# Optimization experiments

Measured on AMD Instinct MI355X. Metric: run time of the kernel, lower is better.

The kernel has to match this reference:

```python
import jax, jax.numpy as jnp
import numpy as np

D_MODEL = 2048
N_HEADS = 16
HEAD_DIM = D_MODEL // N_HEADS
SCALE = HEAD_DIM ** -0.5


def setup_inputs() -> dict:
    key = jax.random.key(0)
    ks = jax.random.split(key, 9)
    B, L, D = 4, 4096, D_MODEL
    s = 1.0 / np.sqrt(D)
    inp = {"x": jax.random.normal(ks[0], (B, L, D), dtype=jnp.float32)}
    inp["Wq"] = jax.random.normal(ks[1], (D, D), dtype=jnp.float32) * s
    inp["bq"] = jnp.zeros((D,), dtype=jnp.float32)
    inp["Wk"] = jax.random.normal(ks[2], (D, D), dtype=jnp.float32) * s
    inp["bk"] = jnp.zeros((D,), dtype=jnp.float32)
    inp["Wv"] = jax.random.normal(ks[3], (D, D), dtype=jnp.float32) * s
    inp["bv"] = jnp.zeros((D,), dtype=jnp.float32)
    inp["Wo"] = jax.random.normal(ks[4], (D, D), dtype=jnp.float32) * s
    inp["bo"] = jnp.zeros((D,), dtype=jnp.float32)
    return inp


def reference(x, Wq, bq, Wk, bk, Wv, bv, Wo, bo):
    B, L, D = x.shape
    H, Hd = N_HEADS, HEAD_DIM
    # projections (torch Linear: x @ W.T + b)
    q = jnp.einsum('bld,ed->ble', x, Wq) + bq
    k = jnp.einsum('bld,ed->ble', x, Wk) + bk
    v = jnp.einsum('bld,ed->ble', x, Wv) + bv
    phi_q = jax.nn.elu(q) + 1.0
    phi_k = jax.nn.elu(k) + 1.0
    # (B, L, H, Hd)
    phi_q = phi_q.reshape(B, L, H, Hd)
    phi_k = phi_k.reshape(B, L, H, Hd)
    v = v.reshape(B, L, H, Hd)
    # elementwise prefix sum over sequence dim
    kv_sum = jnp.cumsum(phi_k * v, axis=1)  # (B, L, H, Hd)
    context = (phi_q * kv_sum).reshape(B, L, D) * SCALE
    return jnp.einsum('bld,ed->ble', context, Wo) + bo
```

## Files before the change

### kernel.cpp

```cpp
#include <hip/hip_runtime.h>
#include <hip/hip_bf16.h>
#include <cstdint>
#include <cstddef>

typedef __bf16 bf16x8 __attribute__((ext_vector_type(8)));
typedef __bf16 bf16x4 __attribute__((ext_vector_type(4)));
typedef float  f32x4  __attribute__((ext_vector_type(4)));

#define D_MODEL 2048
#define SEQ     4096
#define BATCH   4
#define M_TOK   (BATCH * SEQ)
#define ATTN_SCALE 0.08838834764831845f

#define BM 128
#define BN 128
#define BK 64

#define NSEG   64
#define SEGLEN (SEQ / NSEG)

__device__ __forceinline__ void async_load16(const void* g, void* l) {
    __builtin_amdgcn_global_load_lds(
        (const __attribute__((address_space(1))) unsigned int*)g,
        (__attribute__((address_space(3))) unsigned int*)l,
        16, 0, 0);
}

__global__ __launch_bounds__(256) void k_cast_bf16(const float* __restrict__ in,
                                                   __bf16* __restrict__ out,
                                                   int n8) {
    int i = blockIdx.x * 256 + threadIdx.x;
    if (i >= n8) return;
    const float4* in4 = (const float4*)in;
    float4 a = in4[2 * i];
    float4 b = in4[2 * i + 1];
    bf16x8 o;
    o[0] = (__bf16)a.x; o[1] = (__bf16)a.y; o[2] = (__bf16)a.z; o[3] = (__bf16)a.w;
    o[4] = (__bf16)b.x; o[5] = (__bf16)b.y; o[6] = (__bf16)b.z; o[7] = (__bf16)b.w;
    ((bf16x8*)out)[i] = o;
}

__global__ __launch_bounds__(256) void k_cast_w4(const float* __restrict__ w0,
                                                 const float* __restrict__ w1,
                                                 const float* __restrict__ w2,
                                                 const float* __restrict__ w3,
                                                 __bf16* __restrict__ out, int n8) {
    const float* srcs[4] = {w0, w1, w2, w3};
    const float* in = srcs[blockIdx.y];
    __bf16* o = out + (size_t)blockIdx.y * (size_t)n8 * 8;
    int i = blockIdx.x * 256 + threadIdx.x;
    if (i >= n8) return;
    const float4* in4 = (const float4*)in;
    float4 a = in4[2 * i];
    float4 b = in4[2 * i + 1];
    bf16x8 v;
    v[0] = (__bf16)a.x; v[1] = (__bf16)a.y; v[2] = (__bf16)a.z; v[3] = (__bf16)a.w;
    v[4] = (__bf16)b.x; v[5] = (__bf16)b.y; v[6] = (__bf16)b.z; v[7] = (__bf16)b.w;
    ((bf16x8*)o)[i] = v;
}

template <int PHI, typename OUT_T>
__device__ __forceinline__ void gemm_bt(const __bf16* __restrict__ A,
                                        const __bf16* __restrict__ Bm,
                                        const float* __restrict__ bias,
                                        OUT_T* __restrict__ C,
                                        int K, int N) {
    __shared__ __align__(16) __bf16 As[BM * BK];
    __shared__ __align__(16) __bf16 Bs[BN * BK];

    const int tid  = threadIdx.x;
    const int lane = tid & 63;
    const int wave = tid >> 6;
    const int waveM = wave & 1;
    const int waveN = wave >> 1;
    const long bm = (long)blockIdx.y * BM;
    const long bn = (long)blockIdx.x * BN;

    const int srow  = tid >> 3;
    const int sphys = tid & 7;
    const __bf16* gA[4]; const __bf16* gB[4];
    __bf16* lA[4]; __bf16* lB[4];
#pragma unroll
    for (int q = 0; q < 4; q++) {
        int r  = q * 32 + srow;
        int cb = (sphys ^ (r & 7)) * 8;
        gA[q] = A  + (bm + r) * (long)K + cb;
        gB[q] = Bm + (bn + r) * (long)K + cb;
        lA[q] = As + q * 2048 + tid * 8;
        lB[q] = Bs + q * 2048 + tid * 8;
    }

    const int mrow = waveM * 64 + (lane & 15);
    const int nrow = waveN * 64 + (lane & 15);
    const int ksel = lane >> 4;

    f32x4 acc[4][4] = {};

    for (int k0 = 0; k0 < K; k0 += BK) {
#pragma unroll
        for (int q = 0; q < 4; q++) async_load16(gA[q] + k0, lA[q]);
#pragma unroll
        for (int q = 0; q < 4; q++) async_load16(gB[q] + k0, lB[q]);
        __syncthreads();

#pragma unroll
        for (int s = 0; s < 2; s++) {
            bf16x8 af[4], bfr[4];
#pragma unroll
            for (int i = 0; i < 4; i++) {
                int r = mrow + i * 16;
                int p = (s * 4 + ksel) ^ (r & 7);
                af[i] = *(const bf16x8*)(As + r * 64 + p * 8);
            }
#pragma unroll
            for (int j = 0; j < 4; j++) {
                int r = nrow + j * 16;
                int p = (s * 4 + ksel) ^ (r & 7);
                bfr[j] = *(const bf16x8*)(Bs + r * 64 + p * 8);
            }
#pragma unroll
            for (int i = 0; i < 4; i++)
#pragma unroll
                for (int j = 0; j < 4; j++)
                    acc[i][j] = __builtin_amdgcn_mfma_f32_16x16x32_bf16(
                        af[i], bfr[j], acc[i][j], 0, 0, 0);
        }
        __syncthreads();
    }

    const int r0 = (lane >> 4) * 4;
    const int cn = lane & 15;
#pragma unroll
    for (int i = 0; i < 4; i++) {
        long mg = bm + waveM * 64 + i * 16 + r0;
#pragma unroll
        for (int j = 0; j < 4; j++) {
            long ng = bn + waveN * 64 + j * 16 + cn;
            float bia = bias[ng];
#pragma unroll
            for (int r = 0; r < 4; r++) {
                float v = acc[i][j][r] + bia;
                if (PHI) v = (v > 0.f) ? (v + 1.f) : __expf(v);
                C[(mg + r) * (long)N + ng] = (OUT_T)v;
            }
        }
    }
}

__global__ __launch_bounds__(256) void k_gemm_qkv(
    const __bf16* __restrict__ xb,
    const __bf16* __restrict__ wq, const __bf16* __restrict__ wk, const __bf16* __restrict__ wv,
    const float* __restrict__ bq, const float* __restrict__ bk, const float* __restrict__ bv,
    __bf16* __restrict__ oq, __bf16* __restrict__ ok, __bf16* __restrict__ ov) {
    const int z = blockIdx.z;
    const __bf16* W = (z == 0) ? wq : (z == 1) ? wk : wv;
    const float*  b = (z == 0) ? bq : (z == 1) ? bk : bv;
    __bf16*       o = (z == 0) ? oq : (z == 1) ? ok : ov;
    if (z < 2)
        gemm_bt<1, __bf16>(xb, W, b, o, D_MODEL, D_MODEL);
    else
        gemm_bt<0, __bf16>(xb, W, b, o, D_MODEL, D_MODEL);
}

__global__ __launch_bounds__(256) void k_gemm_out(
    const __bf16* __restrict__ ctx, const __bf16* __restrict__ wo,
    const float* __restrict__ bo, float* __restrict__ out) {
    gemm_bt<0, float>(ctx, wo, bo, out, D_MODEL, D_MODEL);
}

__global__ __launch_bounds__(256) void k_scan_partial(
    const __bf16* __restrict__ phik, const __bf16* __restrict__ v,
    float* __restrict__ partial) {
    const int b  = blockIdx.z;
    const int s  = blockIdx.y;
    const int c0 = blockIdx.x * 1024 + threadIdx.x * 4;
    long base = ((long)b * SEQ + (long)s * SEGLEN) * D_MODEL + c0;
    const bf16x4* pk = (const bf16x4*)(phik + base);
    const bf16x4* pv = (const bf16x4*)(v + base);
    float s0 = 0, s1 = 0, s2 = 0, s3 = 0;
    for (int l = 0; l < SEGLEN; l++) {
        bf16x4 a = *pk, w = *pv;
        s0 += (float)a[0] * (float)w[0];
        s1 += (float)a[1] * (float)w[1];
        s2 += (float)a[2] * (float)w[2];
        s3 += (float)a[3] * (float)w[3];
        pk += D_MODEL / 4; pv += D_MODEL / 4;
    }
    *(float4*)(partial + ((long)(b * NSEG + s)) * D_MODEL + c0) = make_float4(s0, s1, s2, s3);
}

__global__ __launch_bounds__(256) void k_scan_apply(
    const __bf16* __restrict__ phiq,
    __bf16* phik_ctx,
    const __bf16* __restrict__ v,
    const float* __restrict__ partial) {
    const int b  = blockIdx.z;
    const int s  = blockIdx.y;
    const int c0 = blockIdx.x * 1024 + threadIdx.x * 4;
    float r0 = 0, r1 = 0, r2 = 0, r3 = 0;
    for (int sp = 0; sp < s; sp++) {
        float4 p = *(const float4*)(partial + ((long)(b * NSEG + sp)) * D_MODEL + c0);
        r0 += p.x; r1 += p.y; r2 += p.z; r3 += p.w;
    }
    long base = ((long)b * SEQ + (long)s * SEGLEN) * D_MODEL + c0;
    bf16x4* pk = (bf16x4*)(phik_ctx + base);
    const bf16x4* pv = (const bf16x4*)(v + base);
    const bf16x4* pq = (const bf16x4*)(phiq + base);
    for (int l = 0; l < SEGLEN; l++) {
        bf16x4 a = *pk, w = *pv, q = *pq;
        r0 += (float)a[0] * (float)w[0];
        r1 += (float)a[1] * (float)w[1];
        r2 += (float)a[2] * (float)w[2];
        r3 += (float)a[3] * (float)w[3];
        bf16x4 o;
        o[0] = (__bf16)((float)q[0] * r0 * ATTN_SCALE);
        o[1] = (__bf16)((float)q[1] * r1 * ATTN_SCALE);
        o[2] = (__bf16)((float)q[2] * r2 * ATTN_SCALE);
        o[3] = (__bf16)((float)q[3] * r3 * ATTN_SCALE);
        *pk = o;
        pk += D_MODEL / 4; pv += D_MODEL / 4; pq += D_MODEL / 4;
    }
}

extern "C" void kernel_launch(void* const* d_in, const int* in_sizes, int n_in,
                              void* d_out, int out_size, void* d_ws, size_t ws_size,
                              hipStream_t stream) {
    const float* x  = (const float*)d_in[0];
    const float* Wq = (const float*)d_in[1];
    const float* bq = (const float*)d_in[2];
    const float* Wk = (const float*)d_in[3];
    const float* bk = (const float*)d_in[4];
    const float* Wv = (const float*)d_in[5];
    const float* bv = (const float*)d_in[6];
    const float* Wo = (const float*)d_in[7];
    const float* bo = (const float*)d_in[8];

    const size_t XB = (size_t)M_TOK * D_MODEL;
    const size_t WB = (size_t)D_MODEL * D_MODEL;

    char* p = (char*)d_ws;
    __bf16* xb   = (__bf16*)p; p += XB * 2;
    __bf16* wqb  = (__bf16*)p; p += WB * 2;
    __bf16* wkb  = (__bf16*)p; p += WB * 2;
    __bf16* wvb  = (__bf16*)p; p += WB * 2;
    __bf16* wob  = (__bf16*)p; p += WB * 2;
    __bf16* phiq = (__bf16*)p; p += XB * 2;
    __bf16* phik = (__bf16*)p; p += XB * 2;
    __bf16* vb   = (__bf16*)p; p += XB * 2;
    if ((size_t)(p - (char*)d_ws) > ws_size) return;

    float*  partial = (float*)xb;
    __bf16* ctx     = phik;

    k_cast_bf16<<<dim3((unsigned)(XB / 8 / 256)), 256, 0, stream>>>(x, xb, (int)(XB / 8));
    k_cast_w4<<<dim3((unsigned)(WB / 8 / 256), 4), 256, 0, stream>>>(Wq, Wk, Wv, Wo, wqb, (int)(WB / 8));

    k_gemm_qkv<<<dim3(D_MODEL / BN, M_TOK / BM, 3), 256, 0, stream>>>(
        xb, wqb, wkb, wvb, bq, bk, bv, phiq, phik, vb);

    k_scan_partial<<<dim3(2, NSEG, BATCH), 256, 0, stream>>>(phik, vb, partial);
    k_scan_apply<<<dim3(2, NSEG, BATCH), 256, 0, stream>>>(phiq, phik, vb, partial);

    k_gemm_out<<<dim3(D_MODEL / BN, M_TOK / BM, 1), 256, 0, stream>>>(
        ctx, wob, bo, (float*)d_out);
}
```

Before: 918.3 us.

## Rewrite GEMMs as 256x256 double-buffered 8-wave pipelined tiles with grid swizzle

Replaces the 128x128 single-buffered GEMM with a 256x256 tile run by 512 threads. It uses 128KB of dynamic LDS for double buffering, and the next tiles' async global-to-LDS loads are interleaved between four MFMA sub-phases, with explicit vmcnt waits, barriers and s_setprio. This aims to hide memory latency behind compute and raise data reuse per tile loaded. A block-index swizzle groups blocks for better L2 locality. In exchange, register pressure and LDS use per block are much higher, which limits occupancy to one block per CU. The hand-tuned waitcnt scheme is fragile.

```diff
diff --git a/kernel.cpp b/kernel.cpp
--- a/kernel.cpp
+++ b/kernel.cpp
@@ -13,9 +13,12 @@
 #define M_TOK   (BATCH * SEQ)
 #define ATTN_SCALE 0.08838834764831845f
 
-#define BM 128
-#define BN 128
+#define BM 256
+#define BN 256
 #define BK 64
+#define NT (D_MODEL / BK)
+#define BUF_BYTES 65536
+#define B_OFF     32768
 
 #define NSEG   64
 #define SEGLEN (SEQ / NSEG)
@@ -26,6 +29,14 @@
         (__attribute__((address_space(3))) unsigned int*)l,
         16, 0, 0);
 }
+
+__device__ __forceinline__ void wg_barrier() {
+    __builtin_amdgcn_sched_barrier(0);
+    __builtin_amdgcn_s_barrier();
+    __builtin_amdgcn_sched_barrier(0);
+}
+
+#define VMCNT(n) asm volatile("s_waitcnt vmcnt(" #n ")" ::: "memory")
 
 __global__ __launch_bounds__(256) void k_cast_bf16(const float* __restrict__ in,
                                                    __bf16* __restrict__ out,
@@ -61,85 +72,114 @@
 }
 
 template <int PHI, typename OUT_T>
-__device__ __forceinline__ void gemm_bt(const __bf16* __restrict__ A,
+__device__ __forceinline__ void gemm256(const __bf16* __restrict__ A,
                                         const __bf16* __restrict__ Bm,
                                         const float* __restrict__ bias,
                                         OUT_T* __restrict__ C,
-                                        int K, int N) {
-    __shared__ __align__(16) __bf16 As[BM * BK];
-    __shared__ __align__(16) __bf16 Bs[BN * BK];
+                                        int bx, int by) {
+    extern __shared__ bf16x8 lds_dyn[];
+    char* lds = (char*)lds_dyn;
 
     const int tid  = threadIdx.x;
     const int lane = tid & 63;
     const int wave = tid >> 6;
-    const int waveM = wave & 1;
-    const int waveN = wave >> 1;
-    const long bm = (long)blockIdx.y * BM;
-    const long bn = (long)blockIdx.x * BN;
-
-    const int srow  = tid >> 3;
-    const int sphys = tid & 7;
-    const __bf16* gA[4]; const __bf16* gB[4];
-    __bf16* lA[4]; __bf16* lB[4];
-#pragma unroll
-    for (int q = 0; q < 4; q++) {
-        int r  = q * 32 + srow;
-        int cb = (sphys ^ (r & 7)) * 8;
-        gA[q] = A  + (bm + r) * (long)K + cb;
-        gB[q] = Bm + (bn + r) * (long)K + cb;
-        lA[q] = As + q * 2048 + tid * 8;
-        lB[q] = Bs + q * 2048 + tid * 8;
-    }
-
-    const int mrow = waveM * 64 + (lane & 15);
-    const int nrow = waveN * 64 + (lane & 15);
+    const int wr = wave & 1;
+    const int wc = wave >> 1;
+    const long bm = (long)by * BM;
+    const long bn = (long)bx * BN;
+    const int  K = D_MODEL, N = D_MODEL;
+
+    const int sp  = tid & 7;
+    const int rA0 = tid >> 3;
+    const int rA1 = 64 + rA0;
+    const int rBe = ((tid >> 8) << 6) + ((tid >> 3) & 31);
+    const int rBo = rBe + 32;
+    const __bf16* gA0 = A  + (bm + rA0) * (long)K + ((sp ^ (rA0 & 7)) << 3);
+    const __bf16* gA1 = A  + (bm + rA1) * (long)K + ((sp ^ (rA1 & 7)) << 3);
+    const __bf16* gBe = Bm + (bn + rBe) * (long)K + ((sp ^ (rBe & 7)) << 3);
+    const __bf16* gBo = Bm + (bn + rBo) * (long)K + ((sp ^ (rBo & 7)) << 3);
+    const long l128K = 128L * K;
+    const int lA0 = tid * 16;
+    const int lA1 = 8192 + tid * 16;
+    const int lBe = B_OFF + ((tid >> 8) << 13) + (((tid >> 3) & 31) << 7) + sp * 16;
+    const int lBo = lBe + 4096;
+
+    auto issue2 = [&](const __bf16* g, int ldsByte) {
+        async_load16(g, lds + ldsByte);
+        async_load16(g + l128K, lds + ldsByte + 16384);
+    };
+
+    issue2(gA0, lA0);              gA0 += BK;
+    issue2(gBe, lBe);              gBe += BK;
+    issue2(gBo, lBo);              gBo += BK;
+    issue2(gA1, lA1);              gA1 += BK;
+    issue2(gA0, lA0 + BUF_BYTES);  gA0 += BK;
+    issue2(gBe, lBe + BUF_BYTES);  gBe += BK;
+    VMCNT(8);
+    wg_barrier();
+
+    const int lm   = lane & 15;
     const int ksel = lane >> 4;
-
-    f32x4 acc[4][4] = {};
-
-    for (int k0 = 0; k0 < K; k0 += BK) {
-#pragma unroll
-        for (int q = 0; q < 4; q++) async_load16(gA[q] + k0, lA[q]);
-#pragma unroll
-        for (int q = 0; q < 4; q++) async_load16(gB[q] + k0, lB[q]);
-        __syncthreads();
-
-#pragma unroll
-        for (int s = 0; s < 2; s++) {
-            bf16x8 af[4], bfr[4];
-#pragma unroll
-            for (int i = 0; i < 4; i++) {
-                int r = mrow + i * 16;
-                int p = (s * 4 + ksel) ^ (r & 7);
-                af[i] = *(const bf16x8*)(As + r * 64 + p * 8);
+    const int m3   = lm & 7;
+    const int clo  = ksel ^ (m3 & 3);
+    const int cb0  = ((((m3 >> 2) << 2) | clo) << 4);
+    const int cb1  = ((((1 ^ (m3 >> 2)) << 2) | clo) << 4);
+    const int aBase = (wr * 128 + lm) * 128;
+    const int bBase = B_OFF + (wc * 64 + lm) * 128;
+
+    f32x4 acc[8][4] = {};
+
+    int cur = 0;
+#pragma unroll 1
+    for (int t = 0; t < NT; ++t) {
+#pragma unroll
+        for (int p = 0; p < 4; ++p) {
+            const int qm = p >> 1, qn = p & 1;
+            bf16x8 af[4][2], bfr[2][2];
+#pragma unroll
+            for (int i = 0; i < 4; ++i) {
+                const char* rp = lds + cur + aBase + (qm * 64 + i * 16) * 128;
+                af[i][0] = *(const bf16x8*)(rp + cb0);
+                af[i][1] = *(const bf16x8*)(rp + cb1);
             }
 #pragma unroll
-            for (int j = 0; j < 4; j++) {
-                int r = nrow + j * 16;
-                int p = (s * 4 + ksel) ^ (r & 7);
-                bfr[j] = *(const bf16x8*)(Bs + r * 64 + p * 8);
+            for (int j = 0; j < 2; ++j) {
+                const char* rp = lds + cur + bBase + (qn * 32 + j * 16) * 128;
+                bfr[j][0] = *(const bf16x8*)(rp + cb0);
+                bfr[j][1] = *(const bf16x8*)(rp + cb1);
             }
-#pragma unroll
-            for (int i = 0; i < 4; i++)
-#pragma unroll
-                for (int j = 0; j < 4; j++)
-                    acc[i][j] = __builtin_amdgcn_mfma_f32_16x16x32_bf16(
-                        af[i], bfr[j], acc[i][j], 0, 0, 0);
+            if (p == 0 && t + 1 < NT) { issue2(gBo, lBo + (cur ^ BUF_BYTES)); gBo += BK; }
+            if (p == 1 && t + 1 < NT) { issue2(gA1, lA1 + (cur ^ BUF_BYTES)); gA1 += BK; }
+            if (p == 2 && t + 2 < NT) { issue2(gA0, lA0 + cur); gA0 += BK; }
+            if (p == 3 && t + 2 < NT) { issue2(gBe, lBe + cur); gBe += BK; }
+            wg_barrier();
+            __builtin_amdgcn_s_setprio(1);
+#pragma unroll
+            for (int s = 0; s < 2; ++s)
+#pragma unroll
+                for (int i = 0; i < 4; ++i)
+#pragma unroll
+                    for (int j = 0; j < 2; ++j)
+                        acc[qm * 4 + i][qn * 2 + j] = __builtin_amdgcn_mfma_f32_16x16x32_bf16(
+                            af[i][s], bfr[j][s], acc[qm * 4 + i][qn * 2 + j], 0, 0, 0);
+            __builtin_amdgcn_s_setprio(0);
+            if (p == 0 || p == 1) { if (t < NT - 1) VMCNT(8); }
+            if (p == 3) { if (t < NT - 2) VMCNT(8); else if (t == NT - 2) VMCNT(0); }
+            wg_barrier();
         }
-        __syncthreads();
-    }
-
-    const int r0 = (lane >> 4) * 4;
-    const int cn = lane & 15;
-#pragma unroll
-    for (int i = 0; i < 4; i++) {
-        long mg = bm + waveM * 64 + i * 16 + r0;
-#pragma unroll
-        for (int j = 0; j < 4; j++) {
-            long ng = bn + waveN * 64 + j * 16 + cn;
-            float bia = bias[ng];
-#pragma unroll
-            for (int r = 0; r < 4; r++) {
+        cur ^= BUF_BYTES;
+    }
+
+    const int r0m = (lane >> 4) << 2;
+#pragma unroll
+    for (int i = 0; i < 8; ++i) {
+        const long mg = bm + wr * 128 + i * 16 + r0m;
+#pragma unroll
+        for (int j = 0; j < 4; ++j) {
+            const long ng = bn + wc * 64 + j * 16 + lm;
+            const float bia = bias[ng];
+#pragma unroll
+            for (int r = 0; r < 4; ++r) {
                 float v = acc[i][j][r] + bia;
                 if (PHI) v = (v > 0.f) ? (v + 1.f) : __expf(v);
                 C[(mg + r) * (long)N + ng] = (OUT_T)v;
@@ -148,25 +188,30 @@
     }
 }
 
-__global__ __launch_bounds__(256) void k_gemm_qkv(
+__global__ __launch_bounds__(512, 2) void k_gemm_qkv(
     const __bf16* __restrict__ xb,
     const __bf16* __restrict__ wq, const __bf16* __restrict__ wk, const __bf16* __restrict__ wv,
     const float* __restrict__ bq, const float* __restrict__ bk, const float* __restrict__ bv,
     __bf16* __restrict__ oq, __bf16* __restrict__ ok, __bf16* __restrict__ ov) {
+    const int flat = blockIdx.y * 8 + blockIdx.x;
+    const int swz  = (flat & 7) * 64 + (flat >> 3);
+    const int bx = swz & 7, by = swz >> 3;
     const int z = blockIdx.z;
     const __bf16* W = (z == 0) ? wq : (z == 1) ? wk : wv;
     const float*  b = (z == 0) ? bq : (z == 1) ? bk : bv;
     __bf16*       o = (z == 0) ? oq : (z == 1) ? ok : ov;
     if (z < 2)
-        gemm_bt<1, __bf16>(xb, W, b, o, D_MODEL, D_MODEL);
+        gemm256<1, __bf16>(xb, W, b, o, bx, by);
     else
-        gemm_bt<0, __bf16>(xb, W, b, o, D_MODEL, D_MODEL);
-}
-
-__global__ __launch_bounds__(256) void k_gemm_out(
+        gemm256<0, __bf16>(xb, W, b, o, bx, by);
+}
+
+__global__ __launch_bounds__(512, 2) void k_gemm_out(
     const __bf16* __restrict__ ctx, const __bf16* __restrict__ wo,
     const float* __restrict__ bo, float* __restrict__ out) {
-    gemm_bt<0, float>(ctx, wo, bo, out, D_MODEL, D_MODEL);
+    const int flat = blockIdx.y * 8 + blockIdx.x;
+    const int swz  = (flat & 7) * 64 + (flat >> 3);
+    gemm256<0, float>(ctx, wo, bo, out, swz & 7, swz >> 3);
 }
 
 __global__ __launch_bounds__(256) void k_scan_partial(
@@ -253,15 +298,24 @@
     float*  partial = (float*)xb;
     __bf16* ctx     = phik;
 
+    static bool attr_done = false;
+    if (!attr_done) {
+        hipFuncSetAttribute(reinterpret_cast<const void*>(&k_gemm_qkv),
+                            hipFuncAttributeMaxDynamicSharedMemorySize, 131072);
+        hipFuncSetAttribute(reinterpret_cast<const void*>(&k_gemm_out),
+                            hipFuncAttributeMaxDynamicSharedMemorySize, 131072);
+        attr_done = true;
+    }
+
     k_cast_bf16<<<dim3((unsigned)(XB / 8 / 256)), 256, 0, stream>>>(x, xb, (int)(XB / 8));
     k_cast_w4<<<dim3((unsigned)(WB / 8 / 256), 4), 256, 0, stream>>>(Wq, Wk, Wv, Wo, wqb, (int)(WB / 8));
 
-    k_gemm_qkv<<<dim3(D_MODEL / BN, M_TOK / BM, 3), 256, 0, stream>>>(
+    k_gemm_qkv<<<dim3(D_MODEL / BN, M_TOK / BM, 3), 512, 131072, stream>>>(
         xb, wqb, wkb, wvb, bq, bk, bv, phiq, phik, vb);
 
     k_scan_partial<<<dim3(2, NSEG, BATCH), 256, 0, stream>>>(phik, vb, partial);
     k_scan_apply<<<dim3(2, NSEG, BATCH), 256, 0, stream>>>(phiq, phik, vb, partial);
 
-    k_gemm_out<<<dim3(D_MODEL / BN, M_TOK / BM, 1), 256, 0, stream>>>(
+    k_gemm_out<<<dim3(D_MODEL / BN, M_TOK / BM, 1), 512, 131072, stream>>>(
         ctx, wob, bo, (float*)d_out);
 }
```

Result: faster. 882.7 us (-3.9%).
